# Optimization experiments

Measured on AMD Instinct MI355X. Metric: run time of the kernel, lower is better.

## Reference

```python
import jax, jax.numpy as jnp
import numpy as np

B, D_DATA, D_DICT0, N_SAE, D_DICT = 2048, 768, 128, 128, 32


def _kaiming_uniform(key, shape, fan_in):
    # torch.nn.init.kaiming_uniform_ default: bound = sqrt(6 / fan_in) / sqrt(5-gain stuff) ~ use gain=sqrt(2)? match torch default a=sqrt(5) not needed; plain kaiming_uniform_ uses gain=sqrt(2): bound = sqrt(6/fan_in)*? Keep simple: bound = sqrt(6.0/fan_in)
    bound = np.sqrt(6.0 / fan_in)
    return jax.random.uniform(key, shape, jnp.float32, -bound, bound)


def setup_inputs() -> dict:
    key = jax.random.key(0)
    ks = jax.random.split(key, 6)
    x = jax.random.normal(ks[0], (B, D_DATA), jnp.float32)
    # top-level SAE params
    W_enc0 = _kaiming_uniform(ks[1], (D_DATA, D_DICT0), D_DATA)
    b_enc0 = jnp.zeros((D_DICT0,), jnp.float32)
    W_dec0 = _kaiming_uniform(ks[2], (D_DICT0, D_DATA), D_DICT0)
    W_dec0 = W_dec0 / jnp.linalg.norm(W_dec0, axis=-1, keepdims=True)
    b_dec0 = jnp.zeros((D_DATA,), jnp.float32)
    # sublayer (hierarchical) per-expert params
    W_enc1 = _kaiming_uniform(ks[3], (N_SAE, D_DATA, D_DICT), D_DATA)
    b_enc1 = jnp.zeros((N_SAE, D_DICT), jnp.float32)
    W_dec1 = _kaiming_uniform(ks[4], (N_SAE, D_DICT, D_DATA), D_DICT)
    W_dec1 = W_dec1 / jnp.linalg.norm(W_dec1, axis=-1, keepdims=True)
    b_dec1 = jnp.zeros((N_SAE, D_DATA), jnp.float32)
    return {"x": x, "W_enc0": W_enc0, "b_enc0": b_enc0, "W_dec0": W_dec0,
            "b_dec0": b_dec0, "W_enc1": W_enc1, "b_enc1": b_enc1,
            "W_dec1": W_dec1, "b_dec1": b_dec1}


def reference(x, W_enc0, b_enc0, W_dec0, b_dec0, W_enc1, b_enc1, W_dec1, b_dec1):
    # ---- sae_0 (standard SAE; scale/unscale are identity) ----
    acts0 = jax.nn.relu((x - b_dec0) @ W_enc0 + b_enc0)        # [B, D_DICT0]
    x0 = acts0 @ W_dec0 + b_dec0                               # [B, D_DATA]
    # ---- binary gate over experts (n_sae == d_dict0) ----
    gate = (acts0 > 0).astype(x.dtype)                         # [B, N_SAE]
    # ---- sublayer: gather-encode-decode-scatter, expressed densely with a
    # binary mask (gate only selects membership; gate value is not multiplied).
    # Avoid materializing [B, N_SAE, D_DATA] by distributing (x - b_dec1[j]):
    pre = (jnp.einsum('bd,jdk->bjk', x, W_enc1)
           - jnp.einsum('jd,jdk->jk', b_dec1, W_enc1)[None]
           + b_enc1[None])                                     # [B, N_SAE, D_DICT]
    acts1 = jax.nn.relu(pre) * gate[:, :, None]                # zero out ungated
    # scatter_add over experts: sum_j gated (acts1[b,j] @ W_dec1[j] + b_dec1[j])
    dec = jnp.einsum('bjk,jkd->bd', acts1, W_dec1) + gate @ b_dec1  # [B, D_DATA]
    return x0 + dec
```

## Files before the change

### kernel.cpp

```cpp
#include <hip/hip_runtime.h>
#include <hip/hip_bf16.h>
#include <stdint.h>

#define B_SZ   2048
#define DDATA  768
#define NSAE   128
#define NJK    4096
#define KA2    4352
#define SPLITK 2
#define KC2    2176
#define GZCH   8
#define GZW    96

typedef unsigned short u16;
typedef short bf16x8 __attribute__((ext_vector_type(8)));
typedef float f32x4  __attribute__((ext_vector_type(4)));

static __device__ __forceinline__ u16 f2bf(float f) {
  __hip_bfloat16 h = __float2bfloat16(f);
  return *reinterpret_cast<u16*>(&h);
}

static __device__ __forceinline__ void gload16(const u16* g, u16* l) {
  __builtin_amdgcn_global_load_lds(
      (const __attribute__((address_space(1))) unsigned int*)g,
      (__attribute__((address_space(3))) unsigned int*)l,
      16, 0, 0);
}

__global__ __launch_bounds__(256) void k_front(const float* __restrict__ x,
                                               const float* __restrict__ We0,
                                               const float* __restrict__ bd0,
                                               const float* __restrict__ We1,
                                               const float* __restrict__ bd1,
                                               const float* __restrict__ be1,
                                               const float* __restrict__ Wd1,
                                               const float* __restrict__ Wd0,
                                               u16* __restrict__ W1T,
                                               float* __restrict__ cv,
                                               u16* __restrict__ B2T,
                                               u16* __restrict__ xb,
                                               float* __restrict__ pp,
                                               float* __restrict__ xnp,
                                               float* __restrict__ wn) {
  __shared__ float smem[64 * 65];
  const int bid = blockIdx.x, t = threadIdx.x;
  if (bid < 128) {
    const int j = bid;
    float* ts  = smem;
    float* bds = smem + 64 * 33;
    float* red = smem + 64 * 33 + 64;
    const int k = t & 31, g = t >> 5;
    float cacc = 0.f;
    for (int db = 0; db < 12; ++db) {
      const float* src = We1 + (size_t)j * 24576 + db * 2048;
#pragma unroll
      for (int i = 0; i < 8; ++i) {
        int e = t + i * 256;
        ts[(e >> 5) * 33 + (e & 31)] = src[e];
      }
      if (t < 64) bds[t] = bd1[(size_t)j * DDATA + db * 64 + t];
      __syncthreads();
#pragma unroll
      for (int i = 0; i < 8; ++i) {
        int e = t + i * 256;
        int kk = e >> 6, d = e & 63;
        W1T[(size_t)(j * 32 + kk) * DDATA + db * 64 + d] = f2bf(ts[d * 33 + kk]);
      }
#pragma unroll
      for (int q = 0; q < 8; ++q) {
        int d = g + 8 * q;
        cacc += ts[d * 33 + k] * bds[d];
      }
      __syncthreads();
    }
    red[g * 32 + k] = cacc;
    __syncthreads();
    if (g == 0) {
      float s = 0.f;
#pragma unroll
      for (int q = 0; q < 8; ++q) s += red[q * 32 + k];
      cv[j * 32 + k] = be1[j * 32 + k] - s;
    }
  } else if (bid < 944) {
    const int e2 = bid - 128;
    const int rb = e2 / 12, dbk = e2 % 12;
    const float* src; int r0, base;
    if (rb < 64)      { src = Wd1; r0 = rb * 64;        base = 0;    }
    else if (rb < 66) { src = Wd0; r0 = (rb - 64) * 64; base = 4096; }
    else              { src = bd1; r0 = (rb - 66) * 64; base = 4224; }
    const int d0 = dbk * 64;
#pragma unroll
    for (int i = 0; i < 16; ++i) {
      int e = t + i * 256;
      int ri = e >> 6, di = e & 63;
      smem[ri * 65 + di] = src[(size_t)(r0 + ri) * DDATA + d0 + di];
    }
    __syncthreads();
#pragma unroll
    for (int i = 0; i < 16; ++i) {
      int e = t + i * 256;
      int di = e >> 6, ri = e & 63;
      B2T[(size_t)(d0 + di) * KA2 + base + r0 + ri] = f2bf(smem[ri * 65 + di]);
    }
  } else if (bid < 952) {
    const int wb = bid - 944;
    const int jj = wb * 16 + (t >> 4), s = t & 15;
    float acc = 0.f;
    for (int d = s; d < DDATA; d += 16) {
      float w = We0[(size_t)d * 128 + jj];
      acc += w * w;
    }
#pragma unroll
    for (int sh = 8; sh; sh >>= 1) acc += __shfl_xor(acc, sh, 64);
    if (s == 0) wn[jj] = sqrtf(acc);
  } else {
    const int bid2 = bid - 952;
    const int b0 = (bid2 & 63) * 32, z = bid2 >> 6;
    const int dbase = z * GZW;
    float* xs = smem;
#pragma unroll
    for (int i = 0; i < 3; ++i) {
      int idx = t + i * 256;
      int r = idx / 24, c4 = idx % 24;
      size_t go = (size_t)(b0 + r) * DDATA + dbase + c4 * 4;
      float4 v = *(const float4*)&x[go];
      ushort4 o;
      o.x = f2bf(v.x); o.y = f2bf(v.y); o.z = f2bf(v.z); o.w = f2bf(v.w);
      *(ushort4*)&xb[go] = o;
      float4 b4 = *(const float4*)&bd0[dbase + c4 * 4];
      v.x -= b4.x; v.y -= b4.y; v.z -= b4.z; v.w -= b4.w;
      *(float4*)&xs[r * GZW + c4 * 4] = v;
    }
    __syncthreads();
    const int jp = t & 63, rg = t >> 6;
    const int j0 = jp * 2;
    float ap[8][2], xq[8];
#pragma unroll
    for (int r = 0; r < 8; ++r) { ap[r][0] = ap[r][1] = xq[r] = 0.f; }
    for (int d = 0; d < GZW; d += 4) {
      float4 xv[8];
#pragma unroll
      for (int r = 0; r < 8; ++r)
        xv[r] = *(const float4*)&xs[(rg * 8 + r) * GZW + d];
#pragma unroll
      for (int dd = 0; dd < 4; ++dd) {
        float2 w2 = *(const float2*)&We0[(size_t)(dbase + d + dd) * 128 + j0];
#pragma unroll
        for (int r = 0; r < 8; ++r) {
          float xr = ((const float*)&xv[r])[dd];
          ap[r][0] += xr * w2.x;
          ap[r][1] += xr * w2.y;
          xq[r]    += xr * xr;
        }
      }
    }
#pragma unroll
    for (int r = 0; r < 8; ++r) {
      size_t o = ((size_t)z * B_SZ + b0 + rg * 8 + r) * 128 + j0;
      *(float2*)&pp[o] = make_float2(ap[r][0], ap[r][1]);
    }
    if (jp == 0) {
#pragma unroll
      for (int r = 0; r < 8; ++r)
        xnp[(size_t)z * B_SZ + b0 + rg * 8 + r] = xq[r];
    }
  }
}

__global__ __launch_bounds__(256) void k_gate2(const float* __restrict__ pp,
                                               const float* __restrict__ xnp,
                                               const float* __restrict__ wn,
                                               const float* __restrict__ be0,
                                               const float* __restrict__ x,
                                               const float* __restrict__ We0,
                                               const float* __restrict__ bd0,
                                               u16* __restrict__ A2) {
  const int i = blockIdx.x * 256 + threadIdx.x;
  const int b = i >> 7, j = i & 127;
  const int lane = threadIdx.x & 63;
  float p = be0[j], xn2 = 0.f;
#pragma unroll
  for (int z = 0; z < GZCH; ++z) {
    p   += pp[((size_t)z * B_SZ + b) * 128 + j];
    xn2 += xnp[(size_t)z * B_SZ + b];
  }
  const float tau = 1e-4f * sqrtf(xn2) * wn[j];
  size_t row = (size_t)b * KA2;
  A2[row + NJK + j]       = f2bf(p > 0.f ? p : 0.f);
  A2[row + NJK + 128 + j] = (p > 0.f) ? (u16)0x3F80 : (u16)0;
  unsigned long long mask = __ballot(fabsf(p) <= tau);
  while (mask) {
    int src = (int)__builtin_ctzll(mask);
    mask &= mask - 1;
    int bb = __shfl(b, src, 64), jj = __shfl(j, src, 64);
    double acc = 0.0;
#pragma unroll
    for (int tt = 0; tt < 12; ++tt) {
      int d = lane + tt * 64;
      acc += (double)(x[(size_t)bb * DDATA + d] - bd0[d]) *
             (double)We0[(size_t)d * 128 + jj];
    }
#pragma unroll
    for (int s = 32; s; s >>= 1) acc += __shfl_xor(acc, s, 64);
    if (lane == src) {
      double pd = acc + (double)be0[jj];
      size_t rw = (size_t)bb * KA2;
      A2[rw + NJK + jj]       = f2bf(pd > 0.0 ? (float)pd : 0.f);
      A2[rw + NJK + 128 + jj] = (pd > 0.0) ? (u16)0x3F80 : (u16)0;
    }
  }
}

template<int BM, int BN, int EPI>
__global__ __launch_bounds__(256) void k_gemm(const u16* __restrict__ A,
                                              const u16* __restrict__ Bm,
                                              int K, int Kc,
                                              float* __restrict__ outF,
                                              u16* __restrict__ A2,
                                              const float* __restrict__ cvec) {
  constexpr int WM = BM / 32, WN = BN / 32;
  __shared__ __align__(16) u16 As[BM * 64];
  __shared__ __align__(16) u16 Bs[BN * 64];
  __shared__ u16 gate_s[BM * 4];
  __shared__ float cv_s[BN];
  const int tid = threadIdx.x;
  const int bx = blockIdx.x, by = blockIdx.y, bz = blockIdx.z;
  const int kbase = bz * Kc;
  const u16* Ab = A  + (size_t)(by * BM) * K;
  const u16* Bb = Bm + (size_t)(bx * BN) * K;
  const int wave = tid >> 6, lane = tid & 63;
  const int wr = wave >> 1, wc = wave & 1;
  const int m0 = wr * (BM / 2), n0 = wc * (BN / 2);
  const int lm = lane & 15, qd = lane >> 4;

  f32x4 acc[WM][WN];
  const f32x4 zero = {0.f, 0.f, 0.f, 0.f};
  for (int mi = 0; mi < WM; ++mi)
    for (int ni = 0; ni < WN; ++ni) acc[mi][ni] = zero;

  for (int k0 = kbase; k0 < kbase + Kc; k0 += 64) {
#pragma unroll
    for (int i = 0; i < BM / 32; ++i) {
      int id = tid + 256 * i;
      int row = id >> 3, u = id & 7;
      gload16(Ab + (size_t)row * K + k0 + ((u ^ (row & 7)) * 8), &As[id * 8]);
    }
#pragma unroll
    for (int i = 0; i < BN / 32; ++i) {
      int id = tid + 256 * i;
      int row = id >> 3, u = id & 7;
      gload16(Bb + (size_t)row * K + k0 + ((u ^ (row & 7)) * 8), &Bs[id * 8]);
    }
    __syncthreads();
#pragma unroll
    for (int s = 0; s < 2; ++s) {
      const int swz = ((s << 2) + qd) ^ (lm & 7);
      bf16x8 af[WM], bfv[WN];
#pragma unroll
      for (int mi = 0; mi < WM; ++mi)
        af[mi] = *(const bf16x8*)&As[(m0 + mi * 16 + lm) * 64 + swz * 8];
#pragma unroll
      for (int ni = 0; ni < WN; ++ni)
        bfv[ni] = *(const bf16x8*)&Bs[(n0 + ni * 16 + lm) * 64 + swz * 8];
#pragma unroll
      for (int mi = 0; mi < WM; ++mi)
#pragma unroll
        for (int ni = 0; ni < WN; ++ni)
          acc[mi][ni] = __builtin_amdgcn_mfma_f32_16x16x32_bf16(af[mi], bfv[ni],
                                                                acc[mi][ni], 0, 0, 0);
    }
    __syncthreads();
  }

  if (EPI == 1) {
    for (int e = tid; e < BM * 4; e += 256) {
      int r = e >> 2, q = e & 3;
      gate_s[e] = A2[(size_t)(by * BM + r) * KA2 + NJK + 128 + bx * 4 + q];
    }
    for (int e = tid; e < BN; e += 256) cv_s[e] = cvec[bx * BN + e];
    __syncthreads();
  }

  const int rb = qd * 4;
#pragma unroll
  for (int mi = 0; mi < WM; ++mi) {
#pragma unroll
    for (int ni = 0; ni < WN; ++ni) {
#pragma unroll
      for (int r = 0; r < 4; ++r) {
        int ml = m0 + mi * 16 + rb + r;
        int nl = n0 + ni * 16 + lm;
        int gm = by * BM + ml;
        int gn = bx * BN + nl;
        float v = acc[mi][ni][r];
        if (EPI == 1) {
          v += cv_s[nl];
          v = v > 0.f ? v : 0.f;
          u16 gbit = gate_s[ml * 4 + (nl >> 5)];
          v = gbit ? v : 0.f;
          float vn = __shfl_xor(v, 1, 64);
          if ((lm & 1) == 0) {
            unsigned pk = (unsigned)f2bf(v) | ((unsigned)f2bf(vn) << 16);
            *(unsigned*)&A2[(size_t)gm * KA2 + gn] = pk;
          }
        } else {
          outF[((size_t)bz * B_SZ + gm) * DDATA + gn] = v;
        }
      }
    }
  }
}

__global__ __launch_bounds__(256) void k_reduce(const float* __restrict__ part,
                                                const float* __restrict__ bias,
                                                float* __restrict__ out) {
  const int N4 = B_SZ * DDATA / 4;
  int i = blockIdx.x * 256 + threadIdx.x;
  const float4* p4 = (const float4*)part;
  float4 s = p4[i];
#pragma unroll
  for (int z = 1; z < SPLITK; ++z) {
    float4 t = p4[i + z * N4];
    s.x += t.x; s.y += t.y; s.z += t.z; s.w += t.w;
  }
  float4 b = ((const float4*)bias)[i % (DDATA / 4)];
  s.x += b.x; s.y += b.y; s.z += b.z; s.w += b.w;
  ((float4*)out)[i] = s;
}

extern "C" void kernel_launch(void* const* d_in, const int* in_sizes, int n_in,
                              void* d_out, int out_size, void* d_ws, size_t ws_size,
                              hipStream_t stream) {
  const float* x   = (const float*)d_in[0];
  const float* We0 = (const float*)d_in[1];
  const float* be0 = (const float*)d_in[2];
  const float* Wd0 = (const float*)d_in[3];
  const float* bd0 = (const float*)d_in[4];
  const float* We1 = (const float*)d_in[5];
  const float* be1 = (const float*)d_in[6];
  const float* Wd1 = (const float*)d_in[7];
  const float* bd1 = (const float*)d_in[8];
  float* out = (float*)d_out;

  uint8_t* ws = (uint8_t*)d_ws;
  size_t off = 0;
  auto carve = [&](size_t bytes) {
    uint8_t* p = ws + off;
    off += (bytes + 255) & ~(size_t)255;
    return p;
  };
  u16*    A2   = (u16*)carve((size_t)B_SZ * KA2 * 2);
  u16*    xb   = (u16*)carve((size_t)B_SZ * DDATA * 2);
  u16*    W1T  = (u16*)carve((size_t)NJK * DDATA * 2);
  u16*    B2T  = (u16*)carve((size_t)DDATA * KA2 * 2);
  float*  cv   = (float*)carve((size_t)NJK * 4);
  float*  part = (float*)carve((size_t)SPLITK * B_SZ * DDATA * 4);
  float*  pp   = (float*)carve((size_t)GZCH * B_SZ * 128 * 4);
  float*  xnp  = (float*)carve((size_t)GZCH * B_SZ * 4);
  float*  wn   = (float*)carve(128 * 4);

  k_front <<<1464, 256, 0, stream>>>(x, We0, bd0, We1, bd1, be1, Wd1, Wd0,
                                     W1T, cv, B2T, xb, pp, xnp, wn);
  k_gate2 <<<1024, 256, 0, stream>>>(pp, xnp, wn, be0, x, We0, bd0, A2);
  k_gemm<128, 128, 1><<<dim3(32, 16, 1), 256, 0, stream>>>(xb, W1T, DDATA, DDATA,
                                                           nullptr, A2, cv);
  k_gemm<64, 128, 2><<<dim3(6, 32, SPLITK), 256, 0, stream>>>(A2, B2T, KA2, KC2,
                                                              part, nullptr, nullptr);
  k_reduce<<<1536, 256, 0, stream>>>(part, bd0, out);
}
```

Baseline: 178.1 us.

## Fuse split-K reduction into GEMM via last-block atomic counter

The separate reduce kernel is removed. Each split-K block of the second GEMM now increments a per-tile counter, and the block that arrives second adds the other half's partial and the bias, then writes the final output. The counters are zeroed by an extra block in the front kernel. The second GEMM's M tile is halved to 32 rows, which doubles its grid. The first GEMM's gate and bias loads move ahead of the main loop so they overlap with it. This trades a kernel launch and a full pass over the partial buffer for atomics, fences and a serialized tail on half the blocks.

```diff
diff --git a/kernel.cpp b/kernel.cpp
--- a/kernel.cpp
+++ b/kernel.cpp
@@ -42,7 +42,8 @@
                                                u16* __restrict__ xb,
                                                float* __restrict__ pp,
                                                float* __restrict__ xnp,
-                                               float* __restrict__ wn) {
+                                               float* __restrict__ wn,
+                                               unsigned int* __restrict__ done) {
   __shared__ float smem[64 * 65];
   const int bid = blockIdx.x, t = threadIdx.x;
   if (bid < 128) {
@@ -114,7 +115,7 @@
 #pragma unroll
     for (int sh = 8; sh; sh >>= 1) acc += __shfl_xor(acc, sh, 64);
     if (s == 0) wn[jj] = sqrtf(acc);
-  } else {
+  } else if (bid < 1464) {
     const int bid2 = bid - 952;
     const int b0 = (bid2 & 63) * 32, z = bid2 >> 6;
     const int dbase = z * GZW;
@@ -165,6 +166,8 @@
       for (int r = 0; r < 8; ++r)
         xnp[(size_t)z * B_SZ + b0 + rg * 8 + r] = xq[r];
     }
+  } else {
+    for (int e = t; e < 384; e += 256) done[e] = 0u;
   }
 }
 
@@ -218,7 +221,10 @@
                                               int K, int Kc,
                                               float* __restrict__ outF,
                                               u16* __restrict__ A2,
-                                              const float* __restrict__ cvec) {
+                                              const float* __restrict__ cvec,
+                                              const float* __restrict__ bias,
+                                              float* __restrict__ outFinal,
+                                              unsigned int* __restrict__ done) {
   constexpr int WM = BM / 32, WN = BN / 32;
   __shared__ __align__(16) u16 As[BM * 64];
   __shared__ __align__(16) u16 Bs[BN * 64];
@@ -234,6 +240,14 @@
   const int m0 = wr * (BM / 2), n0 = wc * (BN / 2);
   const int lm = lane & 15, qd = lane >> 4;
 
+  if (EPI == 1) {
+    for (int e = tid; e < BM * 4; e += 256) {
+      int r = e >> 2, q = e & 3;
+      gate_s[e] = A2[(size_t)(by * BM + r) * KA2 + NJK + 128 + bx * 4 + q];
+    }
+    for (int e = tid; e < BN; e += 256) cv_s[e] = cvec[bx * BN + e];
+  }
+
   f32x4 acc[WM][WN];
   const f32x4 zero = {0.f, 0.f, 0.f, 0.f};
   for (int mi = 0; mi < WM; ++mi)
@@ -270,15 +284,6 @@
           acc[mi][ni] = __builtin_amdgcn_mfma_f32_16x16x32_bf16(af[mi], bfv[ni],
                                                                 acc[mi][ni], 0, 0, 0);
     }
-    __syncthreads();
-  }
-
-  if (EPI == 1) {
-    for (int e = tid; e < BM * 4; e += 256) {
-      int r = e >> 2, q = e & 3;
-      gate_s[e] = A2[(size_t)(by * BM + r) * KA2 + NJK + 128 + bx * 4 + q];
-    }
-    for (int e = tid; e < BN; e += 256) cv_s[e] = cvec[bx * BN + e];
     __syncthreads();
   }
 
@@ -310,23 +315,35 @@
       }
     }
   }
-}
-
-__global__ __launch_bounds__(256) void k_reduce(const float* __restrict__ part,
-                                                const float* __restrict__ bias,
-                                                float* __restrict__ out) {
-  const int N4 = B_SZ * DDATA / 4;
-  int i = blockIdx.x * 256 + threadIdx.x;
-  const float4* p4 = (const float4*)part;
-  float4 s = p4[i];
-#pragma unroll
-  for (int z = 1; z < SPLITK; ++z) {
-    float4 t = p4[i + z * N4];
-    s.x += t.x; s.y += t.y; s.z += t.z; s.w += t.w;
-  }
-  float4 b = ((const float4*)bias)[i % (DDATA / 4)];
-  s.x += b.x; s.y += b.y; s.z += b.z; s.w += b.w;
-  ((float4*)out)[i] = s;
+
+  if (EPI == 2) {
+    __shared__ unsigned int sflag;
+    __syncthreads();
+    if (tid == 0) {
+      __threadfence();
+      sflag = atomicAdd(&done[by * gridDim.x + bx], 1u);
+      __threadfence();
+    }
+    __syncthreads();
+    if (sflag == 1) {
+      const int oz = 1 - bz;
+#pragma unroll
+      for (int mi = 0; mi < WM; ++mi) {
+#pragma unroll
+        for (int ni = 0; ni < WN; ++ni) {
+#pragma unroll
+          for (int r = 0; r < 4; ++r) {
+            int gm = by * BM + m0 + mi * 16 + rb + r;
+            int gn = bx * BN + n0 + ni * 16 + lm;
+            float v = acc[mi][ni][r]
+                    + outF[((size_t)oz * B_SZ + gm) * DDATA + gn]
+                    + bias[gn];
+            outFinal[(size_t)gm * DDATA + gn] = v;
+          }
+        }
+      }
+    }
+  }
 }
 
 extern "C" void kernel_launch(void* const* d_in, const int* in_sizes, int n_in,
@@ -359,13 +376,13 @@
   float*  pp   = (float*)carve((size_t)GZCH * B_SZ * 128 * 4);
   float*  xnp  = (float*)carve((size_t)GZCH * B_SZ * 4);
   float*  wn   = (float*)carve(128 * 4);
-
-  k_front <<<1464, 256, 0, stream>>>(x, We0, bd0, We1, bd1, be1, Wd1, Wd0,
-                                     W1T, cv, B2T, xb, pp, xnp, wn);
+  unsigned int* done = (unsigned int*)carve(384 * 4);
+
+  k_front <<<1465, 256, 0, stream>>>(x, We0, bd0, We1, bd1, be1, Wd1, Wd0,
+                                     W1T, cv, B2T, xb, pp, xnp, wn, done);
   k_gate2 <<<1024, 256, 0, stream>>>(pp, xnp, wn, be0, x, We0, bd0, A2);
-  k_gemm<128, 128, 1><<<dim3(32, 16, 1), 256, 0, stream>>>(xb, W1T, DDATA, DDATA,
-                                                           nullptr, A2, cv);
-  k_gemm<64, 128, 2><<<dim3(6, 32, SPLITK), 256, 0, stream>>>(A2, B2T, KA2, KC2,
-                                                              part, nullptr, nullptr);
-  k_reduce<<<1536, 256, 0, stream>>>(part, bd0, out);
-}
+  k_gemm<128, 128, 1><<<dim3(32, 16, 1), 256, 0, stream>>>(
+      xb, W1T, DDATA, DDATA, nullptr, A2, cv, nullptr, nullptr, nullptr);
+  k_gemm<32, 128, 2><<<dim3(6, 64, SPLITK), 256, 0, stream>>>(
+      A2, B2T, KA2, KC2, part, nullptr, nullptr, bd0, out, done);
+}
```

After: 211.0 us. +18.5%, slower.
